# Performance work log

Hardware: AMD Instinct MI355X
Metric: run time of the kernel (lower is better)

The kernel has to match this reference:

```python
import jax, jax.numpy as jnp
import numpy as np

N = 50000      # nodes
E = 800000     # edges (avg degree 16)
F_IN = 256     # input feature dim
H = 4          # heads
D = 16         # out feats per head
NEG_SLOPE = 0.2


def setup_inputs() -> dict:
    key = jax.random.key(0)
    ks = jax.random.split(key, 8)
    feat = jax.random.normal(ks[0], (N, F_IN), dtype=jnp.float32)
    src = jax.random.randint(ks[1], (E,), 0, N, dtype=jnp.int32)
    dst = jax.random.randint(ks[2], (E,), 0, N, dtype=jnp.int32)
    sc = 1.0 / np.sqrt(F_IN)
    W_src = (jax.random.normal(ks[3], (H * D, F_IN), dtype=jnp.float32) * sc)
    b_src = jnp.zeros((H * D,), dtype=jnp.float32)
    W_dst = (jax.random.normal(ks[4], (H * D, F_IN), dtype=jnp.float32) * sc)
    b_dst = jnp.zeros((H * D,), dtype=jnp.float32)
    attn = jax.random.normal(ks[5], (1, H, D), dtype=jnp.float32) * (1.0 / np.sqrt(D))
    return {"feat": feat, "src": src, "dst": dst, "W_src": W_src,
            "b_src": b_src, "W_dst": W_dst, "b_dst": b_dst, "attn": attn}


def reference(feat, src, dst, W_src, b_src, W_dst, b_dst, attn):
    # Dense projections: [N, H, D]
    feat_src = (feat @ W_src.T + b_src).reshape(N, H, D)
    feat_dst = (feat @ W_dst.T + b_dst).reshape(N, H, D)
    # Gather to edges: [E, H, D]
    el = feat_src[src]
    er = feat_dst[dst]
    e = jax.nn.leaky_relu(el + er, negative_slope=NEG_SLOPE)
    # Per-edge, per-head attention logit: [E, H]
    score = jnp.einsum('ehd,ohd->eh', e, attn)
    # Edge softmax over incoming edges of each destination node
    m = jax.ops.segment_max(score, dst, num_segments=N)          # [N, H]
    a = jnp.exp(score - m[dst])                                  # [E, H]
    s = jax.ops.segment_sum(a, dst, num_segments=N)              # [N, H]
    alpha = a / s[dst]                                           # [E, H]
    # Weighted scatter-aggregate of source features: [N, H, D]
    msg = el * alpha[:, :, None]
    rst = jax.ops.segment_sum(msg, dst, num_segments=N)
    return rst
```

## Files before the change

kernel.cpp:

```cpp
#include <hip/hip_runtime.h>
#include <math.h>

#define NODES 50000
#define EDGES 800000
#define FIN   256
#define HD    64
#define NEG   0.2f

#define PROJ_BLOCKS 782
#define SCAT_BLOCKS 3125
#define PREP_BLOCKS 128
#define HIST_BLOCKS 3125

typedef __attribute__((ext_vector_type(8))) short bf16x8;
typedef __attribute__((ext_vector_type(4))) float f32x4;

__device__ __forceinline__ unsigned pack_hi(unsigned a, unsigned b)
{ return (a >> 16) | (b & 0xFFFF0000u); }

__device__ __forceinline__ void split8(const float4 x01, const float4 x23,
                                       bf16x8& hi, bf16x8& lo)
{
    const float xs[8] = { x01.x, x01.y, x01.z, x01.w, x23.x, x23.y, x23.z, x23.w };
    union { unsigned w[4]; bf16x8 v; } H, L;
#pragma unroll
    for (int p = 0; p < 4; ++p) {
        const float a = xs[2 * p], b = xs[2 * p + 1];
        const unsigned ba = __float_as_uint(a), bb = __float_as_uint(b);
        H.w[p] = pack_hi(ba, bb);
        const float la = a - __uint_as_float(ba & 0xFFFF0000u);
        const float lb = b - __uint_as_float(bb & 0xFFFF0000u);
        L.w[p] = pack_hi(__float_as_uint(la), __float_as_uint(lb));
    }
    hi = H.v; lo = L.v;
}

__global__ void prep_hist_kernel(const float* __restrict__ Wsrc,
                                 const float* __restrict__ Wdst,
                                 short* __restrict__ Bhi, short* __restrict__ Blo,
                                 const int* __restrict__ dst, int* __restrict__ deg)
{
    const int b = blockIdx.x;
    if (b < PREP_BLOCKS) {
        const int i = b * 256 + threadIdx.x;
        const int row = i >> 8, k = i & 255;
        const float x = (row < 64) ? Wsrc[row * FIN + k] : Wdst[(row - 64) * FIN + k];
        const unsigned bb = __float_as_uint(x);
        const float l = x - __uint_as_float(bb & 0xFFFF0000u);
        Bhi[i] = (short)(bb >> 16);
        Blo[i] = (short)(__float_as_uint(l) >> 16);
    } else {
        const int e = (b - PREP_BLOCKS) * 256 + threadIdx.x;
        if (e < EDGES) atomicAdd(&deg[dst[e]], 1);
    }
}

__global__ void scan1_kernel(const int* __restrict__ deg, int* __restrict__ offs,
                             int* __restrict__ part)
{
    __shared__ int lds[256];
    const int t  = threadIdx.x;
    const int i0 = blockIdx.x * 1024 + t * 4;
    int v[4];
#pragma unroll
    for (int k = 0; k < 4; ++k) v[k] = (i0 + k < NODES) ? deg[i0 + k] : 0;
    const int tsum = v[0] + v[1] + v[2] + v[3];
    lds[t] = tsum;
    __syncthreads();
    for (int off = 1; off < 256; off <<= 1) {
        const int x = (t >= off) ? lds[t - off] : 0;
        __syncthreads();
        lds[t] += x;
        __syncthreads();
    }
    const int excl = lds[t] - tsum;
    int run = excl;
#pragma unroll
    for (int k = 0; k < 4; ++k) {
        if (i0 + k < NODES) offs[i0 + k] = run;
        run += v[k];
    }
    if (t == 255) part[blockIdx.x] = lds[255];
}

__global__ void scan3_kernel(int* __restrict__ offs, const int* __restrict__ part,
                             int* __restrict__ cursor)
{
    const int i = blockIdx.x * blockDim.x + threadIdx.x;
    const int pidx = blockIdx.x >> 2;
    int add = 0;
    for (int b = 0; b < pidx; ++b) add += part[b];
    if (i < NODES) {
        const int val = offs[i] + add;
        offs[i]   = val;
        cursor[i] = val;
    }
    if (i == 0) offs[NODES] = EDGES;
}

__global__ __launch_bounds__(256) void proj_scatter_kernel(
    const float* __restrict__ feat,
    const short* __restrict__ Bhi, const short* __restrict__ Blo,
    const float* __restrict__ bsrc, const float* __restrict__ bdst,
    float* __restrict__ fs, float* __restrict__ fd,
    const int* __restrict__ src, const int* __restrict__ dst,
    int* __restrict__ cursor, unsigned short* __restrict__ csr)
{
    __shared__ short sB[2][2][512 * 8];

    if (blockIdx.x >= PROJ_BLOCKS) {
        const int e = (blockIdx.x - PROJ_BLOCKS) * 256 + threadIdx.x;
        if (e < EDGES) {
            const int d   = dst[e];
            const int pos = atomicAdd(&cursor[d], 1);
            csr[pos] = (unsigned short)src[e];
        }
        return;
    }

    const int t    = threadIdx.x;
    const int lane = t & 63;
    const int w    = t >> 6;
    const int fr   = lane & 15;
    const int fq   = lane >> 4;
    const int fragu = fq * 128 + fr;

    const int colu = t & 127;
    const int fq0  = t >> 7;
    const int fq1  = fq0 + 2;

    const int r0 = blockIdx.x * 64 + w * 16;
    int rowA = r0 + fr;  if (rowA >= NODES) rowA = NODES - 1;
    const float* pA = feat + (size_t)rowA * FIN + fq * 8;

    f32x4 acc[8];
#pragma unroll
    for (int n = 0; n < 8; ++n) acc[n] = (f32x4){0.f, 0.f, 0.f, 0.f};

    float4 bs00, bs01, bs10, bs11;
    float4 acA, acB, anA, anB;

#define B_ISSUE(kslice) do {                                                  \
        const size_t o0 = (size_t)colu * FIN + (kslice) * 32 + fq0 * 8;       \
        const size_t o1 = (size_t)colu * FIN + (kslice) * 32 + fq1 * 8;       \
        bs00 = *(const float4*)(Bhi + o0);  bs01 = *(const float4*)(Bhi + o1);\
        bs10 = *(const float4*)(Blo + o0);  bs11 = *(const float4*)(Blo + o1);\
    } while (0)

#define B_WRITE(buf) do {                                                     \
        *(float4*)&sB[buf][0][(size_t)t * 8]         = bs00;                  \
        *(float4*)&sB[buf][0][(size_t)(t + 256) * 8] = bs01;                  \
        *(float4*)&sB[buf][1][(size_t)t * 8]         = bs10;                  \
        *(float4*)&sB[buf][1][(size_t)(t + 256) * 8] = bs11;                  \
    } while (0)

#define A_LOAD(dA, dB, kslice) do {                                           \
        dA = *(const float4*)(pA + (kslice) * 32);                            \
        dB = *(const float4*)(pA + (kslice) * 32 + 4);                        \
    } while (0)

#define COMPUTE(buf, AH, AL) do {                                             \
        _Pragma("unroll")                                                     \
        for (int nf = 0; nf < 8; ++nf) {                                      \
            const bf16x8 bh = *(const bf16x8*)&sB[buf][0][(fragu + nf*16)*8]; \
            const bf16x8 bl = *(const bf16x8*)&sB[buf][1][(fragu + nf*16)*8]; \
            acc[nf] = __builtin_amdgcn_mfma_f32_16x16x32_bf16(AH, bh, acc[nf], 0, 0, 0); \
            acc[nf] = __builtin_amdgcn_mfma_f32_16x16x32_bf16(AL, bh, acc[nf], 0, 0, 0); \
            acc[nf] = __builtin_amdgcn_mfma_f32_16x16x32_bf16(AH, bl, acc[nf], 0, 0, 0); \
        } } while (0)

    B_ISSUE(0);
    A_LOAD(acA, acB, 0);
    B_WRITE(0);
    __syncthreads();

    for (int ks2 = 0; ks2 < 8; ks2 += 2) {
        const int k1 = (ks2 + 1 < 7) ? ks2 + 1 : 7;
        const int k2 = (ks2 + 2 < 7) ? ks2 + 2 : 7;
        bf16x8 ah, al;

        B_ISSUE(k1);
        A_LOAD(anA, anB, k1);
        split8(acA, acB, ah, al);
        COMPUTE(0, ah, al);
        B_WRITE(1);
        __syncthreads();

        B_ISSUE(k2);
        A_LOAD(acA, acB, k2);
        split8(anA, anB, ah, al);
        COMPUTE(1, ah, al);
        B_WRITE(0);
        __syncthreads();
    }

#pragma unroll
    for (int nf = 0; nf < 8; ++nf) {
        float* outp = (nf < 4) ? fs : fd;
        const float bias = ((nf < 4) ? bsrc : bdst)[(nf & 3) * 16 + fr];
        const int c = (nf & 3) * 16 + fr;
#pragma unroll
        for (int r = 0; r < 4; ++r) {
            const int row = r0 + fq * 4 + r;
            if (row < NODES)
                outp[(size_t)row * HD + c] = acc[nf][r] + bias;
        }
    }
#undef B_ISSUE
#undef B_WRITE
#undef A_LOAD
#undef COMPUTE
}

__device__ __forceinline__ float head_sum16(float x)
{
    x += __int_as_float(__builtin_amdgcn_update_dpp(0, __float_as_int(x), 0xB1,  0xf, 0xf, true));
    x += __int_as_float(__builtin_amdgcn_update_dpp(0, __float_as_int(x), 0x4E,  0xf, 0xf, true));
    x += __int_as_float(__builtin_amdgcn_update_dpp(0, __float_as_int(x), 0x141, 0xf, 0xf, true));
    x += __int_as_float(__builtin_amdgcn_update_dpp(0, __float_as_int(x), 0x140, 0xf, 0xf, true));
    return x;
}

__global__ __launch_bounds__(256) void gat_kernel(
    const float* __restrict__ fs, const float* __restrict__ fd,
    const float* __restrict__ attn,
    const int* __restrict__ offs, const unsigned short* __restrict__ csr,
    float* __restrict__ out)
{
    const int wid  = (blockIdx.x * blockDim.x + threadIdx.x) >> 6;
    const int lane = threadIdx.x & 63;
    if (wid >= NODES) return;

    const float er = fd[(size_t)wid * HD + lane];
    const float aw = attn[lane];
    const int start = __builtin_amdgcn_readfirstlane(offs[wid]);
    const int end   = __builtin_amdgcn_readfirstlane(offs[wid + 1]);

    float s = 0.f, acc = 0.f;

    for (int base = start; base < end; base += 64) {
        const int rem = end - base;
        const int cnt = rem < 64 ? rem : 64;
        int srcv = 0;
        if (lane < cnt) srcv = (int)csr[base + lane];

        int j = 0;
        for (; j + 4 <= cnt; j += 4) {
            const int i0 = __builtin_amdgcn_readlane(srcv, j + 0);
            const int i1 = __builtin_amdgcn_readlane(srcv, j + 1);
            const int i2 = __builtin_amdgcn_readlane(srcv, j + 2);
            const int i3 = __builtin_amdgcn_readlane(srcv, j + 3);
            const float el0 = fs[(size_t)i0 * HD + lane];
            const float el1 = fs[(size_t)i1 * HD + lane];
            const float el2 = fs[(size_t)i2 * HD + lane];
            const float el3 = fs[(size_t)i3 * HD + lane];
            const float t0 = el0 + er, t1 = el1 + er, t2 = el2 + er, t3 = el3 + er;
            const float e0 = fmaf(NEG, fminf(t0, 0.f), fmaxf(t0, 0.f));
            const float e1 = fmaf(NEG, fminf(t1, 0.f), fmaxf(t1, 0.f));
            const float e2 = fmaf(NEG, fminf(t2, 0.f), fmaxf(t2, 0.f));
            const float e3 = fmaf(NEG, fminf(t3, 0.f), fmaxf(t3, 0.f));
            const float p0 = head_sum16(e0 * aw);
            const float p1 = head_sum16(e1 * aw);
            const float p2 = head_sum16(e2 * aw);
            const float p3 = head_sum16(e3 * aw);
            const float pe0 = __expf(p0);
            const float pe1 = __expf(p1);
            const float pe2 = __expf(p2);
            const float pe3 = __expf(p3);
            s += (pe0 + pe1) + (pe2 + pe3);
            acc = fmaf(pe0, el0, fmaf(pe1, el1, fmaf(pe2, el2, fmaf(pe3, el3, acc))));
        }
        for (; j < cnt; ++j) {
            const int i0 = __builtin_amdgcn_readlane(srcv, j);
            const float el0 = fs[(size_t)i0 * HD + lane];
            const float t0 = el0 + er;
            const float e0 = fmaf(NEG, fminf(t0, 0.f), fmaxf(t0, 0.f));
            const float pe0 = __expf(head_sum16(e0 * aw));
            s += pe0;
            acc = fmaf(pe0, el0, acc);
        }
    }
    out[(size_t)wid * HD + lane] = (end > start) ? (acc / s) : 0.f;
}

extern "C" void kernel_launch(void* const* d_in, const int* in_sizes, int n_in,
                              void* d_out, int out_size, void* d_ws, size_t ws_size,
                              hipStream_t stream)
{
    const float* feat = (const float*)d_in[0];
    const int*   src  = (const int*)  d_in[1];
    const int*   dst  = (const int*)  d_in[2];
    const float* Wsrc = (const float*)d_in[3];
    const float* bsrc = (const float*)d_in[4];
    const float* Wdst = (const float*)d_in[5];
    const float* bdst = (const float*)d_in[6];
    const float* attn = (const float*)d_in[7];
    float* out = (float*)d_out;

    float* fs     = (float*)d_ws;
    float* fd     = fs + (size_t)NODES * HD;
    int*   offs   = (int*)(fd + (size_t)NODES * HD);
    int*   deg    = offs + (NODES + 16);
    int*   cursor = deg + NODES;
    int*   part   = cursor + NODES;
    unsigned short* csr = (unsigned short*)(part + 64);
    short* Bhi    = (short*)(csr + EDGES);
    short* Blo    = Bhi + 128 * FIN;

    const int scan_blocks = (NODES + 1023) / 1024;

    hipMemsetAsync(deg, 0, NODES * sizeof(int), stream);

    prep_hist_kernel<<<PREP_BLOCKS + HIST_BLOCKS, 256, 0, stream>>>(
        Wsrc, Wdst, Bhi, Blo, dst, deg);
    scan1_kernel<<<scan_blocks, 256, 0, stream>>>(deg, offs, part);
    scan3_kernel<<<(NODES + 255) / 256, 256, 0, stream>>>(offs, part, cursor);
    proj_scatter_kernel<<<PROJ_BLOCKS + SCAT_BLOCKS, 256, 0, stream>>>(
        feat, Bhi, Blo, bsrc, bdst, fs, fd, src, dst, cursor, csr);
    gat_kernel<<<((size_t)NODES * 64 + 255) / 256, 256, 0, stream>>>(
        fs, fd, attn, offs, csr, out);
}
```

Measured before the change: 242.9 us.

## Replace per-edge global atomic CSR scatter with two-level bucketed scatter

Edges are no longer scattered into CSR with one global atomic per edge. A staging pass builds per-block LDS histograms over 256-node buckets, reserves bucket ranges with one global atomic per bucket, and writes packed (src, local dst) words. A new bucket_scatter kernel then places edges within each bucket using LDS atomics. This is meant to cut global atomic contention and random writes, at the cost of an extra kernel launch and an extra pass over the edges through global memory.

```diff
diff --git a/kernel.cpp b/kernel.cpp
--- a/kernel.cpp
+++ b/kernel.cpp
@@ -8,7 +8,8 @@
 #define NEG   0.2f
 
 #define PROJ_BLOCKS 782
-#define SCAT_BLOCKS 3125
+#define NB          196
+#define STAGE_BLOCKS 196
 #define PREP_BLOCKS 128
 #define HIST_BLOCKS 3125
 
@@ -84,7 +85,7 @@
 }
 
 __global__ void scan3_kernel(int* __restrict__ offs, const int* __restrict__ part,
-                             int* __restrict__ cursor)
+                             int* __restrict__ bcur)
 {
     const int i = blockIdx.x * blockDim.x + threadIdx.x;
     const int pidx = blockIdx.x >> 2;
@@ -92,33 +93,54 @@
     for (int b = 0; b < pidx; ++b) add += part[b];
     if (i < NODES) {
         const int val = offs[i] + add;
-        offs[i]   = val;
-        cursor[i] = val;
+        offs[i] = val;
+        if ((i & 255) == 0) bcur[i >> 8] = val;
     }
     if (i == 0) offs[NODES] = EDGES;
 }
 
-__global__ __launch_bounds__(256) void proj_scatter_kernel(
+__global__ __launch_bounds__(256) void proj_stage_kernel(
     const float* __restrict__ feat,
     const short* __restrict__ Bhi, const short* __restrict__ Blo,
     const float* __restrict__ bsrc, const float* __restrict__ bdst,
     float* __restrict__ fs, float* __restrict__ fd,
     const int* __restrict__ src, const int* __restrict__ dst,
-    int* __restrict__ cursor, unsigned short* __restrict__ csr)
+    int* __restrict__ bcur, unsigned* __restrict__ bedge)
 {
     __shared__ short sB[2][2][512 * 8];
+    __shared__ int   sH[NB], sBase[NB];
+
+    const int t = threadIdx.x;
 
     if (blockIdx.x >= PROJ_BLOCKS) {
-        const int e = (blockIdx.x - PROJ_BLOCKS) * 256 + threadIdx.x;
-        if (e < EDGES) {
-            const int d   = dst[e];
-            const int pos = atomicAdd(&cursor[d], 1);
-            csr[pos] = (unsigned short)src[e];
+        const int e0 = (blockIdx.x - PROJ_BLOCKS) * 4096;
+        for (int i = t; i < NB; i += 256) sH[i] = 0;
+        __syncthreads();
+#pragma unroll
+        for (int k = 0; k < 16; ++k) {
+            const int e = e0 + k * 256 + t;
+            if (e < EDGES) atomicAdd(&sH[dst[e] >> 8], 1);
+        }
+        __syncthreads();
+        for (int i = t; i < NB; i += 256) {
+            const int c = sH[i];
+            sBase[i] = c ? atomicAdd(&bcur[i], c) : 0;
+            sH[i] = 0;
+        }
+        __syncthreads();
+#pragma unroll
+        for (int k = 0; k < 16; ++k) {
+            const int e = e0 + k * 256 + t;
+            if (e < EDGES) {
+                const int d = dst[e];
+                const int b = d >> 8;
+                const int p = sBase[b] + atomicAdd(&sH[b], 1);
+                bedge[p] = (unsigned)src[e] | ((unsigned)(d & 255) << 16);
+            }
         }
         return;
     }
 
-    const int t    = threadIdx.x;
     const int lane = t & 63;
     const int w    = t >> 6;
     const int fr   = lane & 15;
@@ -210,6 +232,26 @@
 #undef B_WRITE
 #undef A_LOAD
 #undef COMPUTE
+}
+
+__global__ __launch_bounds__(256) void bucket_scatter_kernel(
+    const int* __restrict__ offs, const unsigned* __restrict__ bedge,
+    unsigned short* __restrict__ csr)
+{
+    __shared__ int cur[256];
+    const int b  = blockIdx.x;
+    const int t  = threadIdx.x;
+    const int n0 = b * 256;
+    const int start = offs[n0];
+    const int node  = n0 + t;
+    cur[t] = ((node < NODES) ? offs[node] : EDGES) - start;
+    __syncthreads();
+    const int end = (n0 + 256 <= NODES) ? offs[n0 + 256] : EDGES;
+    for (int i = start + t; i < end; i += 256) {
+        const unsigned pk = bedge[i];
+        const int rel = atomicAdd(&cur[(pk >> 16) & 255], 1);
+        csr[start + rel] = (unsigned short)(pk & 0xFFFFu);
+    }
 }
 
 __device__ __forceinline__ float head_sum16(float x)
@@ -301,9 +343,10 @@
     float* fd     = fs + (size_t)NODES * HD;
     int*   offs   = (int*)(fd + (size_t)NODES * HD);
     int*   deg    = offs + (NODES + 16);
-    int*   cursor = deg + NODES;
-    int*   part   = cursor + NODES;
-    unsigned short* csr = (unsigned short*)(part + 64);
+    int*   part   = deg + NODES;
+    int*   bcur   = part + 64;
+    unsigned* bedge = (unsigned*)(bcur + 256);
+    unsigned short* csr = (unsigned short*)(bedge + EDGES);
     short* Bhi    = (short*)(csr + EDGES);
     short* Blo    = Bhi + 128 * FIN;
 
@@ -314,9 +357,10 @@
     prep_hist_kernel<<<PREP_BLOCKS + HIST_BLOCKS, 256, 0, stream>>>(
         Wsrc, Wdst, Bhi, Blo, dst, deg);
     scan1_kernel<<<scan_blocks, 256, 0, stream>>>(deg, offs, part);
-    scan3_kernel<<<(NODES + 255) / 256, 256, 0, stream>>>(offs, part, cursor);
-    proj_scatter_kernel<<<PROJ_BLOCKS + SCAT_BLOCKS, 256, 0, stream>>>(
-        feat, Bhi, Blo, bsrc, bdst, fs, fd, src, dst, cursor, csr);
+    scan3_kernel<<<(NODES + 255) / 256, 256, 0, stream>>>(offs, part, bcur);
+    proj_stage_kernel<<<PROJ_BLOCKS + STAGE_BLOCKS, 256, 0, stream>>>(
+        feat, Bhi, Blo, bsrc, bdst, fs, fd, src, dst, bcur, bedge);
+    bucket_scatter_kernel<<<NB, 256, 0, stream>>>(offs, bedge, csr);
     gat_kernel<<<((size_t)NODES * 64 + 255) / 256, 256, 0, stream>>>(
         fs, fd, attn, offs, csr, out);
 }
```

Measured after the change: 223.5 us. -8.0%, faster.
